# Kernel optimization log

Hardware: AMD Instinct MI355X
Metric: run time of the kernel (lower is better)

## Reference

```python
import jax, jax.numpy as jnp
import numpy as np

B, L, D, E, H = 4, 2048, 512, 8, 1024

def setup_inputs() -> dict:
    key = jax.random.key(0)
    k1, k2, k3, k4 = jax.random.split(key, 4)
    x = jax.random.normal(k1, (B, L, D), dtype=jnp.float32)
    weights = jax.random.uniform(k2, (B, L, E), dtype=jnp.float32)
    w1 = jax.random.normal(k3, (E, D, H), dtype=jnp.float32) * 0.02
    b1 = jnp.zeros((E, H), dtype=jnp.float32)
    w2 = jax.random.normal(k4, (E, H, D), dtype=jnp.float32) * 0.02
    b2 = jnp.zeros((E, D), dtype=jnp.float32)
    return {"x": x, "weights": weights, "w1": w1, "b1": b1, "w2": w2, "b2": b2}

def reference(x, weights, w1, b1, w2, b2):
    # h: [B, L, E, H]
    h = jnp.einsum('bld,edh->bleh', x, w1) + b1[None, None, :, :]
    h = jax.nn.gelu(h, approximate=False)  # torch F.gelu default is exact (erf)
    # out: [B, L, E, D]
    out = jnp.einsum('bleh,ehd->bled', h, w2) + b2[None, None, :, :]
    # weighted sum over experts -> [B, L, D]
    return jnp.einsum('bled,ble->bld', out, weights)
```

## Files before the change

kernel.cpp:

```cpp
#include <hip/hip_runtime.h>
#include <hip/hip_bf16.h>

#define DEV __device__ __forceinline__

typedef __bf16 bf16;
typedef __bf16 bf16x4 __attribute__((ext_vector_type(4)));
typedef __bf16 bf16x8 __attribute__((ext_vector_type(8)));
typedef float f32x4 __attribute__((ext_vector_type(4)));

static constexpr int Bb = 4, Ll = 2048, Dd = 512, Ee = 8, Hh = 1024;
static constexpr int Mm = Bb * Ll;
static constexpr int GKS = Ee * Hh;
static constexpr int TSZ = 65536;

DEV void gload_lds16(const void* g, void* l) {
  __builtin_amdgcn_global_load_lds(
      (const __attribute__((address_space(1))) unsigned int*)g,
      (__attribute__((address_space(3))) unsigned int*)l, 16, 0, 0);
}

DEV float gelu_fast(float h) {
  const float k = 0.7978845608028654f * 2.0f * 1.4426950408889634f;
  float h2 = h * h;
  float y = h * (k + (0.044715f * k) * h2);
  float t = exp2f(y);
  return h - h * __frcp_rn(t + 1.0f);
}

__global__ void cvt_x_kernel(const float* __restrict__ in, bf16* __restrict__ out, int n4) {
  int i = blockIdx.x * blockDim.x + threadIdx.x;
  if (i < n4) {
    float4 v = ((const float4*)in)[i];
    bf16x4 o = {(bf16)v.x, (bf16)v.y, (bf16)v.z, (bf16)v.w};
    ((bf16x4*)out)[i] = o;
  }
}

__global__ void transpose_cvt(const float* __restrict__ in, bf16* __restrict__ out,
                              int R, int C, size_t in_es, size_t out_es, int out_rs) {
  __shared__ float tile[64][65];
  const int e = blockIdx.z;
  const float* ip = in + (size_t)e * in_es;
  bf16* op = out + (size_t)e * out_es;
  const int r0 = blockIdx.y * 64, c0 = blockIdx.x * 64;
  const int tc = threadIdx.x & 63, tr = threadIdx.x >> 6;
#pragma unroll
  for (int i = 0; i < 16; ++i) {
    const int r = tr + i * 4;
    tile[r][tc] = ip[(size_t)(r0 + r) * C + c0 + tc];
  }
  __syncthreads();
  const int wr = threadIdx.x & 63, wc0 = threadIdx.x >> 6;
#pragma unroll
  for (int i = 0; i < 16; ++i) {
    const int c = wc0 + i * 4;
    op[(size_t)(c0 + c) * out_rs + r0 + wr] = (bf16)tile[wr][c];
  }
}

#define PIPE_DECLS                                                   \
  const int t = threadIdx.x;                                         \
  const int lane = t & 63;                                           \
  const int wid = t >> 6;                                            \
  const int wm = wid >> 2, wn = wid & 3;                             \
  const int fr = lane & 15, fg = lane >> 4, fq = lane >> 4;          \
  const int srow = t >> 2;                                           \
  const int sq = (t & 3) ^ ((t >> 3) & 3);                           \
  const int rsl = fg ^ ((fr >> 1) & 3);

#define PHASE0(buf)                                                  \
  bf16x8 bfr[4], af[4];                                              \
  _Pragma("unroll") for (int fj = 0; fj < 4; ++fj) {                 \
    const int row = wn * 64 + fj * 16 + fr;                          \
    bfr[fj] = *(const bf16x8*)((buf) + 16384 + row * 64 + rsl * 16); \
  }                                                                  \
  _Pragma("unroll") for (int fi = 0; fi < 4; ++fi) {                 \
    const int row = wm * 128 + fi * 16 + fr;                         \
    af[fi] = *(const bf16x8*)((buf) + row * 64 + rsl * 16);          \
  }

#define PHASE1_READS(buf)                                            \
  bf16x8 af2[4];                                                     \
  _Pragma("unroll") for (int fi = 0; fi < 4; ++fi) {                 \
    const int row = wm * 128 + (4 + fi) * 16 + fr;                   \
    af2[fi] = *(const bf16x8*)((buf) + row * 64 + rsl * 16);         \
  }

#define MFMA_CLUSTER(A, ACCOFF)                                      \
  __builtin_amdgcn_s_barrier();                                      \
  asm volatile("s_waitcnt lgkmcnt(0)" ::: "memory");                 \
  __builtin_amdgcn_sched_barrier(0);                                 \
  __builtin_amdgcn_s_setprio(1);                                     \
  _Pragma("unroll") for (int fi = 0; fi < 4; ++fi)                   \
  _Pragma("unroll") for (int fj = 0; fj < 4; ++fj)                   \
    acc[(ACCOFF) + fi][fj] = __builtin_amdgcn_mfma_f32_16x16x32_bf16(\
        bfr[fj], (A)[fi], acc[(ACCOFF) + fi][fj], 0, 0, 0);          \
  __builtin_amdgcn_s_setprio(0);

__global__ __launch_bounds__(512, 1) void ffn_stage1_f(
    const bf16* __restrict__ xb, const bf16* __restrict__ w1t,
    const float* __restrict__ b1, const float* __restrict__ wts,
    bf16* __restrict__ G) {
  __shared__ __align__(16) char lds[98304];
  __shared__ float b1s[1024];
  __shared__ float wls[256];
  const int mt = blockIdx.x, e = blockIdx.y;
  PIPE_DECLS
  b1s[t] = b1[e * Hh + t];
  b1s[512 + t] = b1[e * Hh + 512 + t];
  if (t < 256) wls[t] = wts[((size_t)mt * 256 + t) * Ee + e];

  const bf16* Ag = xb + (size_t)mt * 256 * Dd;
  const bf16* Bg0 = w1t + (size_t)e * Hh * Dd;

  auto stageA = [&](int it, char* buf) {
    const int k0 = (it & 15) * 32;
    gload_lds16(Ag + (size_t)srow * Dd + k0 + sq * 8, buf + wid * 1024);
    gload_lds16(Ag + (size_t)(128 + srow) * Dd + k0 + sq * 8, buf + 8192 + wid * 1024);
  };
  auto stageB = [&](int it, char* buf) {
    const bf16* Bg = Bg0 + (size_t)(it >> 4) * 256 * Dd;
    const int k0 = (it & 15) * 32;
    gload_lds16(Bg + (size_t)srow * Dd + k0 + sq * 8, buf + 16384 + wid * 1024);
    gload_lds16(Bg + (size_t)(128 + srow) * Dd + k0 + sq * 8, buf + 24576 + wid * 1024);
  };

  f32x4 acc[8][4] = {};
  const int NT = 64;
  stageA(0, lds); stageB(0, lds);
  stageA(1, lds + 32768); stageB(1, lds + 32768);
  for (int it = 0; it < NT; ++it) {
    char* buf = lds + (it % 3) * 32768;
    char* nbuf = lds + ((it + 2) % 3) * 32768;
    if (it + 1 < NT) {
      asm volatile("s_waitcnt vmcnt(4)" ::: "memory");
    } else {
      asm volatile("s_waitcnt vmcnt(0)" ::: "memory");
    }
    __builtin_amdgcn_s_barrier();
    {
      PHASE0(buf)
      if (it + 2 < NT) stageA(it + 2, nbuf);
      MFMA_CLUSTER(af, 0)
      PHASE1_READS(buf)
      if (it + 2 < NT) stageB(it + 2, nbuf);
      MFMA_CLUSTER(af2, 4)
    }
    if ((it & 15) == 15) {
      const int ct = it >> 4;
      bf16* tbase = G + ((((size_t)e * 32 + mt) * 4) + ct) * TSZ;
      float b1v[4][4];
#pragma unroll
      for (int fj = 0; fj < 4; ++fj)
#pragma unroll
        for (int r = 0; r < 4; ++r)
          b1v[fj][r] = b1s[ct * 256 + wn * 64 + fj * 16 + fq * 4 + r];
#pragma unroll
      for (int fi = 0; fi < 8; ++fi) {
        const int mp = wm * 128 + fi * 16 + fr;
        const float wgt = wls[mp];
        bf16* gp = tbase + (size_t)mp * 256 + wn * 64 + fq * 4;
#pragma unroll
        for (int fj = 0; fj < 4; ++fj) {
          bf16x4 o;
#pragma unroll
          for (int r = 0; r < 4; ++r) {
            float v = acc[fi][fj][r] + b1v[fj][r];
            o[r] = (bf16)(gelu_fast(v) * wgt);
          }
          *(bf16x4*)(gp + fj * 16) = o;
#pragma unroll
          for (int r = 0; r < 4; ++r) acc[fi][fj][r] = 0.f;
        }
      }
    }
  }
}

__global__ __launch_bounds__(512, 1) void ffn_stage2_f(
    const bf16* __restrict__ G, const bf16* __restrict__ w2t,
    float* __restrict__ P, int eslabs) {
  __shared__ __align__(16) char lds[98304];
  const int mt = blockIdx.x, nt = blockIdx.y, s = blockIdx.z;
  PIPE_DECLS
  const bf16* Bg = w2t + (size_t)nt * 256 * GKS + (size_t)s * eslabs * Hh;

  auto stageA = [&](int it, char* buf) {
    const int eidx = s * eslabs + (it >> 5);
    const int ct = (it >> 3) & 3;
    const int hp = (it & 7) * 32;
    const bf16* tb = G + ((((size_t)eidx * 32 + mt) * 4) + ct) * TSZ;
    gload_lds16(tb + (size_t)srow * 256 + hp + sq * 8, buf + wid * 1024);
    gload_lds16(tb + (size_t)(128 + srow) * 256 + hp + sq * 8, buf + 8192 + wid * 1024);
  };
  auto stageB = [&](int it, char* buf) {
    const int k0 = it * 32;
    gload_lds16(Bg + (size_t)srow * GKS + k0 + sq * 8, buf + 16384 + wid * 1024);
    gload_lds16(Bg + (size_t)(128 + srow) * GKS + k0 + sq * 8, buf + 24576 + wid * 1024);
  };

  f32x4 acc[8][4] = {};
  const int NT = eslabs * 32;
  stageA(0, lds); stageB(0, lds);
  stageA(1, lds + 32768); stageB(1, lds + 32768);
  for (int it = 0; it < NT; ++it) {
    char* buf = lds + (it % 3) * 32768;
    char* nbuf = lds + ((it + 2) % 3) * 32768;
    if (it + 1 < NT) {
      asm volatile("s_waitcnt vmcnt(4)" ::: "memory");
    } else {
      asm volatile("s_waitcnt vmcnt(0)" ::: "memory");
    }
    __builtin_amdgcn_s_barrier();
    {
      PHASE0(buf)
      if (it + 2 < NT) stageA(it + 2, nbuf);
      MFMA_CLUSTER(af, 0)
      PHASE1_READS(buf)
      if (it + 2 < NT) stageB(it + 2, nbuf);
      MFMA_CLUSTER(af2, 4)
    }
  }

  float* Pp = P + (size_t)s * Mm * Dd;
#pragma unroll
  for (int fi = 0; fi < 8; ++fi) {
    const size_t m = (size_t)mt * 256 + wm * 128 + fi * 16 + fr;
    float* pp = Pp + m * Dd + nt * 256 + wn * 64 + fq * 4;
#pragma unroll
    for (int fj = 0; fj < 4; ++fj) *(f32x4*)(pp + fj * 16) = acc[fi][fj];
  }
}

__global__ __launch_bounds__(256) void reduce_bias(
    const float* __restrict__ P, const float* __restrict__ wts,
    const float* __restrict__ b2, float* __restrict__ out, int S) {
  const int n4 = Mm * Dd / 4;
  int i = blockIdx.x * 256 + threadIdx.x;
  if (i >= n4) return;
  const int m = i / (Dd / 4);
  const int d0 = (i % (Dd / 4)) * 4;
  float4 a = ((const float4*)P)[i];
  for (int s = 1; s < S; ++s) {
    float4 p = ((const float4*)P)[(size_t)s * n4 + i];
    a.x += p.x; a.y += p.y; a.z += p.z; a.w += p.w;
  }
  const float* wr = wts + (size_t)m * Ee;
#pragma unroll
  for (int e = 0; e < Ee; ++e) {
    const float w = wr[e];
    float4 b = *(const float4*)(b2 + e * Dd + d0);
    a.x += w * b.x; a.y += w * b.y; a.z += w * b.z; a.w += w * b.w;
  }
  ((float4*)out)[i] = a;
}

extern "C" void kernel_launch(void* const* d_in, const int* in_sizes, int n_in,
                              void* d_out, int out_size, void* d_ws, size_t ws_size,
                              hipStream_t stream) {
  const float* x   = (const float*)d_in[0];
  const float* wts = (const float*)d_in[1];
  const float* w1  = (const float*)d_in[2];
  const float* b1  = (const float*)d_in[3];
  const float* w2  = (const float*)d_in[4];
  const float* b2  = (const float*)d_in[5];
  float* out = (float*)d_out;

  char* ws = (char*)d_ws;
  size_t off = 0;
  bf16* xb  = (bf16*)(ws + off); off += (size_t)Mm * Dd * 2;
  bf16* w1t = (bf16*)(ws + off); off += (size_t)Ee * Hh * Dd * 2;
  bf16* w2t = (bf16*)(ws + off); off += (size_t)Dd * Ee * Hh * 2;

  const size_t gfull = (size_t)Mm * Ee * Hh * 2;
  const size_t psz   = (size_t)Mm * Dd * 4;

  cvt_x_kernel<<<(Mm * Dd / 4 + 255) / 256, 256, 0, stream>>>(x, xb, Mm * Dd / 4);
  transpose_cvt<<<dim3(Hh / 64, Dd / 64, Ee), 256, 0, stream>>>(
      w1, w1t, Dd, Hh, (size_t)Dd * Hh, (size_t)Hh * Dd, Dd);
  transpose_cvt<<<dim3(Dd / 64, Hh / 64, Ee), 256, 0, stream>>>(
      w2, w2t, Hh, Dd, (size_t)Hh * Dd, (size_t)Hh, Ee * Hh);

  int S = 0;
  if (ws_size >= off + gfull + 4 * psz) S = 4;
  else if (ws_size >= off + gfull + 2 * psz) S = 2;

  if (S >= 2) {
    bf16* G = (bf16*)(ws + off);
    float* P = (float*)(ws + off + gfull);
    ffn_stage1_f<<<dim3(Mm / 256, Ee), 512, 0, stream>>>(
        xb, w1t, b1, wts, G);
    ffn_stage2_f<<<dim3(Mm / 256, Dd / 256, S), 512, 0, stream>>>(
        G, w2t, P, Ee / S);
    reduce_bias<<<(Mm * Dd / 4 + 255) / 256, 256, 0, stream>>>(P, wts, b2, out, S);
  }
}
```

Before: 225.1 us.

## Defer stage-1 epilogue stores and spread them across next tile's K loop

The stage-1 kernel now computes the GELU/weight epilogue into a bf16 register buffer at the end of each output column tile. It then issues those global stores two at a time inside the following tile's 16 K-iterations instead of storing them all in one burst. The vmcnt wait counts are adjusted to account for the interleaved stores. The aim is to overlap epilogue store traffic with MFMA work and global-to-LDS loads. The cost is 64 extra VGPRs for the held outputs, which could hurt register pressure.

Result: slower. 268.5 us (+19.3%).

```diff
diff --git a/kernel.cpp b/kernel.cpp
--- a/kernel.cpp
+++ b/kernel.cpp
@@ -126,55 +126,65 @@
   };
 
   f32x4 acc[8][4] = {};
-  const int NT = 64;
+  bf16x4 gout[8][4];
+  bf16* gprev = G;
   stageA(0, lds); stageB(0, lds);
   stageA(1, lds + 32768); stageB(1, lds + 32768);
-  for (int it = 0; it < NT; ++it) {
-    char* buf = lds + (it % 3) * 32768;
-    char* nbuf = lds + ((it + 2) % 3) * 32768;
-    if (it + 1 < NT) {
-      asm volatile("s_waitcnt vmcnt(4)" ::: "memory");
-    } else {
-      asm volatile("s_waitcnt vmcnt(0)" ::: "memory");
-    }
-    __builtin_amdgcn_s_barrier();
-    {
+
+  for (int ct = 0; ct < 4; ++ct) {
+#pragma unroll
+    for (int kt = 0; kt < 16; ++kt) {
+      const int it = ct * 16 + kt;
+      if (ct == 0 || (ct == 1 && kt == 0)) {
+        asm volatile("s_waitcnt vmcnt(4)" ::: "memory");
+      } else if (ct == 3 && kt == 15) {
+        asm volatile("s_waitcnt vmcnt(2)" ::: "memory");
+      } else {
+        asm volatile("s_waitcnt vmcnt(6)" ::: "memory");
+      }
+      __builtin_amdgcn_s_barrier();
+      if (ct > 0) {
+        *(bf16x4*)(gprev + (kt >> 1) * 4096 + ((kt & 1) * 2) * 16) =
+            gout[kt >> 1][(kt & 1) * 2];
+        *(bf16x4*)(gprev + (kt >> 1) * 4096 + ((kt & 1) * 2 + 1) * 16) =
+            gout[kt >> 1][(kt & 1) * 2 + 1];
+      }
+      char* buf = lds + (it % 3) * 32768;
+      char* nbuf = lds + ((it + 2) % 3) * 32768;
       PHASE0(buf)
-      if (it + 2 < NT) stageA(it + 2, nbuf);
+      if (it + 2 < 64) stageA(it + 2, nbuf);
       MFMA_CLUSTER(af, 0)
       PHASE1_READS(buf)
-      if (it + 2 < NT) stageB(it + 2, nbuf);
+      if (it + 2 < 64) stageB(it + 2, nbuf);
       MFMA_CLUSTER(af2, 4)
     }
-    if ((it & 15) == 15) {
-      const int ct = it >> 4;
-      bf16* tbase = G + ((((size_t)e * 32 + mt) * 4) + ct) * TSZ;
-      float b1v[4][4];
-#pragma unroll
-      for (int fj = 0; fj < 4; ++fj)
-#pragma unroll
-        for (int r = 0; r < 4; ++r)
-          b1v[fj][r] = b1s[ct * 256 + wn * 64 + fj * 16 + fq * 4 + r];
-#pragma unroll
-      for (int fi = 0; fi < 8; ++fi) {
-        const int mp = wm * 128 + fi * 16 + fr;
-        const float wgt = wls[mp];
-        bf16* gp = tbase + (size_t)mp * 256 + wn * 64 + fq * 4;
-#pragma unroll
-        for (int fj = 0; fj < 4; ++fj) {
-          bf16x4 o;
-#pragma unroll
-          for (int r = 0; r < 4; ++r) {
-            float v = acc[fi][fj][r] + b1v[fj][r];
-            o[r] = (bf16)(gelu_fast(v) * wgt);
-          }
-          *(bf16x4*)(gp + fj * 16) = o;
-#pragma unroll
-          for (int r = 0; r < 4; ++r) acc[fi][fj][r] = 0.f;
+    bf16* tbase = G + ((((size_t)e * 32 + mt) * 4) + ct) * TSZ;
+    gprev = tbase + ((size_t)(wm * 128 + fr)) * 256 + wn * 64 + fq * 4;
+    float b1v[4][4];
+#pragma unroll
+    for (int fj = 0; fj < 4; ++fj)
+#pragma unroll
+      for (int r = 0; r < 4; ++r)
+        b1v[fj][r] = b1s[ct * 256 + wn * 64 + fj * 16 + fq * 4 + r];
+#pragma unroll
+    for (int fi = 0; fi < 8; ++fi) {
+      const float wgt = wls[wm * 128 + fi * 16 + fr];
+#pragma unroll
+      for (int fj = 0; fj < 4; ++fj) {
+#pragma unroll
+        for (int r = 0; r < 4; ++r) {
+          float v = acc[fi][fj][r] + b1v[fj][r];
+          gout[fi][fj][r] = (bf16)(gelu_fast(v) * wgt);
+          acc[fi][fj][r] = 0.f;
         }
       }
     }
   }
+#pragma unroll
+  for (int fi = 0; fi < 8; ++fi)
+#pragma unroll
+    for (int fj = 0; fj < 4; ++fj)
+      *(bf16x4*)(gprev + fi * 4096 + fj * 16) = gout[fi][fj];
 }
 
 __global__ __launch_bounds__(512, 1) void ffn_stage2_f(
```
